# Performance work log

Hardware: AMD Instinct MI355X
Metric: run time of the kernel (lower is better)

Reference implementation:

```python
import jax, jax.numpy as jnp
import numpy as np

N_NODES = 300000   # cell instances
N_NETS  = 200000   # hyperedges (nets); each net has exactly one source/driver
E_SINK  = 1000000  # sink (node->net) pin edges
NODE_DIM, NET_DIM, EMB = 32, 16, 64
L, NUM_VN = 3, 1000
OUT_NODE, OUT_NET = 4, 4
SLOPE = 0.01  # torch leaky_relu default negative_slope


def leaky(x):
    return jnp.where(x >= 0, x, SLOPE * x)


def _lin(key, fan_in, fan_out):
    kw, kb = jax.random.split(key)
    b = 1.0 / np.sqrt(fan_in)
    W = jax.random.uniform(kw, (fan_in, fan_out), jnp.float32, -b, b)
    bb = jax.random.uniform(kb, (fan_out,), jnp.float32, -b, b)
    return W, bb


def setup_inputs() -> dict:
    key = jax.random.key(0)
    ks = iter(jax.random.split(key, 64))
    d = {}
    d["node_features"] = jax.random.normal(next(ks), (N_NODES, NODE_DIM), jnp.float32)
    d["net_features"] = jax.random.normal(next(ks), (N_NETS, NET_DIM), jnp.float32)
    d["src_nodes"] = jax.random.randint(next(ks), (N_NETS,), 0, N_NODES)   # driver node of net i
    d["sink_nodes"] = jax.random.randint(next(ks), (E_SINK,), 0, N_NODES)
    d["sink_nets"] = jax.random.randint(next(ks), (E_SINK,), 0, N_NETS)
    d["edge_weight"] = jax.random.uniform(next(ks), (E_SINK,), jnp.float32)
    d["batch"] = jax.random.randint(next(ks), (N_NODES,), 0, NUM_VN)       # node -> virtual node id
    # node / net encoders
    d["ne_W1"], d["ne_b1"] = _lin(next(ks), NODE_DIM, 2 * EMB)
    d["ne_W2"], d["ne_b2"] = _lin(next(ks), 2 * EMB, EMB)
    d["te_W1"], d["te_b1"] = _lin(next(ks), NET_DIM, EMB)
    d["te_W2"], d["te_b2"] = _lin(next(ks), EMB, EMB)
    d["vn_emb"] = jnp.zeros((EMB,), jnp.float32)  # torch: init.constant_(weight, 0)
    # HyperConv layers, stacked over L
    Wnet, bnet, Wnode, bnode = [], [], [], []
    for _ in range(L):
        W, b = _lin(next(ks), 3 * EMB, EMB); Wnet.append(W); bnet.append(b)
        W, b = _lin(next(ks), 2 * EMB, EMB); Wnode.append(W); bnode.append(b)
    d["conv_Wnet"] = jnp.stack(Wnet); d["conv_bnet"] = jnp.stack(bnet)
    d["conv_Wnode"] = jnp.stack(Wnode); d["conv_bnode"] = jnp.stack(bnode)
    # virtual-node MLPs (L-1 of them)
    vW1, vb1, vW2, vb2 = [], [], [], []
    for _ in range(L - 1):
        W, b = _lin(next(ks), EMB, EMB); vW1.append(W); vb1.append(b)
        W, b = _lin(next(ks), EMB, EMB); vW2.append(W); vb2.append(b)
    d["vn_W1"] = jnp.stack(vW1); d["vn_b1"] = jnp.stack(vb1)
    d["vn_W2"] = jnp.stack(vW2); d["vn_b2"] = jnp.stack(vb2)
    # output heads
    d["fc1n_W"], d["fc1n_b"] = _lin(next(ks), EMB, 256)
    d["fc2n_W"], d["fc2n_b"] = _lin(next(ks), 256, OUT_NODE)
    d["fc1e_W"], d["fc1e_b"] = _lin(next(ks), EMB, 64)
    d["fc2e_W"], d["fc2e_b"] = _lin(next(ks), 64, OUT_NET)
    return d


def _forward(node_features, net_features, edge_weight,
             ne_W1, ne_b1, ne_W2, ne_b2, te_W1, te_b1, te_W2, te_b2,
             vn_emb, conv_Wnet, conv_bnet, conv_Wnode, conv_bnode,
             vn_W1, vn_b1, vn_W2, vn_b2,
             fc1n_W, fc1n_b, fc2n_W, fc2n_b, fc1e_W, fc1e_b, fc2e_W, fc2e_b,
             src_nodes, sink_nodes, sink_nets, batch):
    h = leaky(node_features @ ne_W1 + ne_b1) @ ne_W2 + ne_b2   # [N, EMB]
    g = leaky(net_features @ te_W1 + te_b1) @ te_W2 + te_b2    # [M, EMB]
    w = edge_weight[:, None]
    vn = jnp.broadcast_to(vn_emb, (NUM_VN, EMB))               # embedding of all-zero indices
    for l in range(L):
        h = h + vn[batch]
        # node -> net (hyperedge) aggregation: driver message + weighted sink sum
        agg_src = h[src_nodes]                                             # [M, EMB]
        agg_sink = jax.ops.segment_sum(h[sink_nodes] * w, sink_nets, num_segments=N_NETS)
        g = jnp.concatenate([g, agg_src, agg_sink], axis=-1) @ conv_Wnet[l] + conv_bnet[l]
        # net -> node aggregation
        back = jax.ops.segment_sum(g, src_nodes, num_segments=N_NODES) \
             + jax.ops.segment_sum(g[sink_nets] * w, sink_nodes, num_segments=N_NODES)
        h = jnp.concatenate([h, back], axis=-1) @ conv_Wnode[l] + conv_bnode[l]
        h = leaky(h)
        g = leaky(g)
        if l < L - 1:
            pooled = jax.ops.segment_max(h, batch, num_segments=NUM_VN)   # global_max_pool
            tmp = pooled + vn
            vn = vn + (leaky(tmp @ vn_W1[l] + vn_b1[l]) @ vn_W2[l] + vn_b2[l])
    node_rep = jnp.abs(leaky(h @ fc1n_W + fc1n_b) @ fc2n_W + fc2n_b)
    net_rep = jnp.abs(leaky(g @ fc1e_W + fc1e_b) @ fc2e_W + fc2e_b)
    return node_rep, net_rep


def reference(node_features, net_features, edge_weight,
              ne_W1, ne_b1, ne_W2, ne_b2, te_W1, te_b1, te_W2, te_b2,
              vn_emb, conv_Wnet, conv_bnet, conv_Wnode, conv_bnode,
              vn_W1, vn_b1, vn_W2, vn_b2,
              fc1n_W, fc1n_b, fc2n_W, fc2n_b, fc1e_W, fc1e_b, fc2e_W, fc2e_b,
              src_nodes, sink_nodes, sink_nets, batch):
    return _forward(node_features, net_features, edge_weight,
                    ne_W1, ne_b1, ne_W2, ne_b2, te_W1, te_b1, te_W2, te_b2,
                    vn_emb, conv_Wnet, conv_bnet, conv_Wnode, conv_bnode,
                    vn_W1, vn_b1, vn_W2, vn_b2,
                    fc1n_W, fc1n_b, fc2n_W, fc2n_b, fc1e_W, fc1e_b, fc2e_W, fc2e_b,
                    src_nodes, sink_nodes, sink_nets, batch)
```

## Files before the change

### kernel.cpp

```cpp
#include <hip/hip_runtime.h>
#include <cstdint>

static constexpr int N_NODES = 300000;
static constexpr int N_NETS  = 200000;
static constexpr int E_SINK  = 1000000;
static constexpr int NODE_DIM = 32;
static constexpr int NET_DIM  = 16;
static constexpr int EMB = 64;
static constexpr int NUM_VN = 1000;
#define SLOPE 0.01f

typedef __attribute__((ext_vector_type(8))) short bhalf8;
typedef __attribute__((ext_vector_type(4))) float floatx4;
typedef unsigned short u16;

__device__ __forceinline__ float leaky(float x) { return x >= 0.f ? x : SLOPE * x; }

__device__ __forceinline__ unsigned bf16_rne(float x) {
    unsigned u = __float_as_uint(x);
    return (u + 0x7FFFu + ((u >> 16) & 1u)) >> 16;
}
__device__ __forceinline__ void split1(float x, u16& hh, u16& ll) {
    unsigned hb = bf16_rne(x);
    float fh = __uint_as_float(hb << 16);
    unsigned lb = bf16_rne(x - fh);
    hh = (u16)hb; ll = (u16)lb;
}

__device__ __forceinline__ void csplit8(const float* x, bhalf8& ah, bhalf8& al) {
#pragma unroll
    for (int e = 0; e < 8; ++e) {
        unsigned u = __float_as_uint(x[e]);
        ah[e] = (short)(u >> 16);
        float d = x[e] - __uint_as_float(u & 0xFFFF0000u);
        al[e] = (short)(__float_as_uint(d) >> 16);
    }
}
template<bool LK>
__device__ __forceinline__ void afrag32(const float* rowp, int kbase, bhalf8& ah, bhalf8& al) {
    float4 v0 = *(const float4*)(rowp + kbase);
    float4 v1 = *(const float4*)(rowp + kbase + 4);
    float x[8] = {v0.x, v0.y, v0.z, v0.w, v1.x, v1.y, v1.z, v1.w};
    if (LK) {
#pragma unroll
        for (int e = 0; e < 8; ++e) x[e] = leaky(x[e]);
    }
    csplit8(x, ah, al);
}
__device__ __forceinline__ void afragl(const float* tp, bhalf8& ah, bhalf8& al) {
    float4 v0 = *(const float4*)tp;
    float4 v1 = *(const float4*)(tp + 4);
    float x[8] = {v0.x, v0.y, v0.z, v0.w, v1.x, v1.y, v1.z, v1.w};
    csplit8(x, ah, al);
}

__device__ __forceinline__ floatx4 mm3(bhalf8 ah, bhalf8 al, bhalf8 wh, bhalf8 wl, floatx4 c) {
    c = __builtin_amdgcn_mfma_f32_16x16x32_bf16(ah, wh, c, 0, 0, 0);
    c = __builtin_amdgcn_mfma_f32_16x16x32_bf16(ah, wl, c, 0, 0, 0);
    c = __builtin_amdgcn_mfma_f32_16x16x32_bf16(al, wh, c, 0, 0, 0);
    return c;
}

static constexpr int OFF_NEW1 = 0;
static constexpr int OFF_NEW2 = 4096;
static constexpr int OFF_TEW1 = 12288;
static constexpr int OFF_TEW2 = 14336;
static constexpr int OFF_CWNET = 18432;
static constexpr int OFF_CWNODE = 55296;
static constexpr int OFF_FC1N = 79872;
static constexpr int OFF_FC1E = 96256;
static constexpr int W_TOTAL  = 100352;

__global__ void k_prep_w(const float* __restrict__ neW1, const float* __restrict__ neW2,
                         const float* __restrict__ teW1, const float* __restrict__ teW2,
                         const float* __restrict__ cWnet, const float* __restrict__ cWnode,
                         const float* __restrict__ fc1n, const float* __restrict__ fc1e,
                         u16* __restrict__ wfh, u16* __restrict__ wfl)
{
    int i = blockIdx.x * 256 + threadIdx.x;
    if (i >= W_TOTAL) return;
    int r, ncols, K; const float* src;
    if (i < OFF_NEW2)        { r = i;             src = neW1;  ncols = 128; K = 32; }
    else if (i < OFF_TEW1)   { r = i - OFF_NEW2;  src = neW2;  ncols = 64;  K = 128; }
    else if (i < OFF_TEW2)   { r = i - OFF_TEW1;  src = teW1;  ncols = 64;  K = 16; }
    else if (i < OFF_CWNET)  { r = i - OFF_TEW2;  src = teW2;  ncols = 64;  K = 64; }
    else if (i < OFF_CWNODE) { int t = i - OFF_CWNET;  int l = t / 12288; r = t % 12288;
                               src = cWnet + (size_t)l * 192 * 64; ncols = 64; K = 192; }
    else if (i < OFF_FC1N)   { int t = i - OFF_CWNODE; int l = t / 8192;  r = t % 8192;
                               src = cWnode + (size_t)l * 128 * 64; ncols = 64; K = 128; }
    else if (i < OFF_FC1E)   { r = i - OFF_FC1N;  src = fc1n;  ncols = 256; K = 64; }
    else                     { r = i - OFF_FC1E;  src = fc1e;  ncols = 64;  K = 64; }
    int e = r & 7, g = (r >> 3) & 3;
    int cidx = r >> 5;
    int col = cidx % ncols, kt = cidx / ncols;
    int k = kt * 32 + g * 8 + e;
    float v = (k < K) ? src[(size_t)k * ncols + col] : 0.f;
    u16 hh, ll; split1(v, hh, ll);
    wfh[i] = hh; wfl[i] = ll;
}

__device__ __forceinline__ bhalf8 ldw(const u16* p, int idx) {
    return *(const bhalf8*)(p + idx);
}

__global__ void k_hist_edges(const int* __restrict__ sink_nets, const int* __restrict__ sink_nodes,
                             int* __restrict__ cnt_net, int* __restrict__ cnt_node)
{
    int e = blockIdx.x * 256 + threadIdx.x;
    if (e >= E_SINK) return;
    atomicAdd(&cnt_net[sink_nets[e]], 1);
    atomicAdd(&cnt_node[sink_nodes[e]], 1);
}

__global__ void k_hist_misc(const int* __restrict__ src_nodes, const int* __restrict__ batch,
                            int* __restrict__ cnt_src, int* __restrict__ cnt_vn)
{
    int i = blockIdx.x * 256 + threadIdx.x;
    if (i < N_NETS) atomicAdd(&cnt_src[src_nodes[i]], 1);
    if (i < N_NODES) atomicAdd(&cnt_vn[batch[i]], 1);
}

__global__ void k_scan1(const int* __restrict__ cnt, int n, int* __restrict__ bsum) {
    __shared__ int s[256];
    int i = blockIdx.x * 256 + threadIdx.x;
    s[threadIdx.x] = (i < n) ? cnt[i] : 0;
    __syncthreads();
    for (int off = 128; off; off >>= 1) {
        if (threadIdx.x < off) s[threadIdx.x] += s[threadIdx.x + off];
        __syncthreads();
    }
    if (threadIdx.x == 0) bsum[blockIdx.x] = s[0];
}

__global__ void k_scan2(int* __restrict__ data, int n) {
    __shared__ int s[256];
    __shared__ int carry_s;
    int tid = threadIdx.x;
    if (tid == 0) carry_s = 0;
    __syncthreads();
    for (int base = 0; base < n; base += 256) {
        int i = base + tid;
        int v = (i < n) ? data[i] : 0;
        s[tid] = v;
        __syncthreads();
        for (int off = 1; off < 256; off <<= 1) {
            int t = (tid >= off) ? s[tid - off] : 0;
            __syncthreads();
            s[tid] += t;
            __syncthreads();
        }
        int excl = s[tid] - v + carry_s;
        if (i < n) data[i] = excl;
        __syncthreads();
        if (tid == 255) carry_s = excl + v;
        __syncthreads();
    }
}

__global__ void k_scan3(const int* __restrict__ cnt, int n, const int* __restrict__ bsum,
                        int* __restrict__ start) {
    __shared__ int s[256];
    int i = blockIdx.x * 256 + threadIdx.x;
    int v = (i < n) ? cnt[i] : 0;
    s[threadIdx.x] = v;
    __syncthreads();
    for (int off = 1; off < 256; off <<= 1) {
        int t = (threadIdx.x >= off) ? s[threadIdx.x - off] : 0;
        __syncthreads();
        s[threadIdx.x] += t;
        __syncthreads();
    }
    int excl = s[threadIdx.x] - v + bsum[blockIdx.x];
    if (i < n) start[i] = excl;
    if (i == n - 1) start[n] = excl + v;
}

__global__ void k_fill_edges(const int* __restrict__ sink_nets, const int* __restrict__ sink_nodes,
                             const float* __restrict__ ew,
                             const int* __restrict__ net_start, const int* __restrict__ node_start,
                             int* __restrict__ cur_net, int* __restrict__ cur_node,
                             int2* __restrict__ e_pack, int2* __restrict__ e2_pack)
{
    int e = blockIdx.x * 256 + threadIdx.x;
    if (e >= E_SINK) return;
    int tn = sink_nets[e], dn = sink_nodes[e];
    int wbits = __float_as_int(ew[e]);
    int p = net_start[tn] + atomicAdd(&cur_net[tn], 1);
    e_pack[p] = make_int2(dn, wbits);
    int q = node_start[dn] + atomicAdd(&cur_node[dn], 1);
    e2_pack[q] = make_int2(tn, wbits);
}

__global__ void k_fill_misc(const int* __restrict__ src_nodes, const int* __restrict__ batch,
                            const int* __restrict__ src_start, const int* __restrict__ vn_start,
                            int* __restrict__ cur_src, int* __restrict__ cur_vn,
                            int* __restrict__ s_net, int* __restrict__ b_node)
{
    int i = blockIdx.x * 256 + threadIdx.x;
    if (i < N_NETS) {
        int d = src_nodes[i];
        int p = src_start[d] + atomicAdd(&cur_src[d], 1);
        s_net[p] = i;
    }
    if (i < N_NODES) {
        int v = batch[i];
        int p = vn_start[v] + atomicAdd(&cur_vn[v], 1);
        b_node[p] = i;
    }
}

__global__ __launch_bounds__(256) void k_gather_agg(
    float* __restrict__ agg, const float* __restrict__ h,
    const int* __restrict__ net_start, const int2* __restrict__ e_pack)
{
    int w = (blockIdx.x * 256 + threadIdx.x) >> 6;
    if (w >= N_NETS) return;
    int lane = threadIdx.x & 63;
    int grp = lane >> 3, l8 = lane & 7;
    int j0 = net_start[w], j1 = net_start[w + 1];
    float a[8] = {0.f, 0.f, 0.f, 0.f, 0.f, 0.f, 0.f, 0.f};
    for (int j = j0 + grp; j < j1; j += 8) {
        int2 pk = e_pack[j];
        float wt = __int_as_float(pk.y);
        const float4* rp = (const float4*)(h + (size_t)pk.x * 64 + l8 * 8);
        float4 v0 = rp[0], v1 = rp[1];
        a[0] += wt * v0.x; a[1] += wt * v0.y; a[2] += wt * v0.z; a[3] += wt * v0.w;
        a[4] += wt * v1.x; a[5] += wt * v1.y; a[6] += wt * v1.z; a[7] += wt * v1.w;
    }
#pragma unroll
    for (int e = 0; e < 8; ++e) {
        a[e] += __shfl_xor(a[e], 8, 64);
        a[e] += __shfl_xor(a[e], 16, 64);
        a[e] += __shfl_xor(a[e], 32, 64);
    }
    if (grp == 0) {
        float4* op = (float4*)(agg + (size_t)w * 64 + l8 * 8);
        op[0] = make_float4(a[0], a[1], a[2], a[3]);
        op[1] = make_float4(a[4], a[5], a[6], a[7]);
    }
}

__global__ __launch_bounds__(256) void k_gather_back(
    float* __restrict__ back, const float* __restrict__ g,
    const int* __restrict__ src_start, const int* __restrict__ s_net,
    const int* __restrict__ node_start, const int2* __restrict__ e2_pack)
{
    int w = (blockIdx.x * 256 + threadIdx.x) >> 6;
    if (w >= N_NODES) return;
    int lane = threadIdx.x & 63;
    int grp = lane >> 3, l8 = lane & 7;
    float a[8] = {0.f, 0.f, 0.f, 0.f, 0.f, 0.f, 0.f, 0.f};
    int j0 = src_start[w], j1 = src_start[w + 1];
    for (int j = j0 + grp; j < j1; j += 8) {
        int idx = s_net[j];
        const float4* rp = (const float4*)(g + (size_t)idx * 64 + l8 * 8);
        float4 v0 = rp[0], v1 = rp[1];
        a[0] += v0.x; a[1] += v0.y; a[2] += v0.z; a[3] += v0.w;
        a[4] += v1.x; a[5] += v1.y; a[6] += v1.z; a[7] += v1.w;
    }
    j0 = node_start[w]; j1 = node_start[w + 1];
    for (int j = j0 + grp; j < j1; j += 8) {
        int2 pk = e2_pack[j];
        float wt = __int_as_float(pk.y);
        const float4* rp = (const float4*)(g + (size_t)pk.x * 64 + l8 * 8);
        float4 v0 = rp[0], v1 = rp[1];
        a[0] += wt * v0.x; a[1] += wt * v0.y; a[2] += wt * v0.z; a[3] += wt * v0.w;
        a[4] += wt * v1.x; a[5] += wt * v1.y; a[6] += wt * v1.z; a[7] += wt * v1.w;
    }
#pragma unroll
    for (int e = 0; e < 8; ++e) {
        a[e] += __shfl_xor(a[e], 8, 64);
        a[e] += __shfl_xor(a[e], 16, 64);
        a[e] += __shfl_xor(a[e], 32, 64);
    }
    if (grp == 0) {
        float4* op = (float4*)(back + (size_t)w * 64 + l8 * 8);
        op[0] = make_float4(a[0], a[1], a[2], a[3]);
        op[1] = make_float4(a[4], a[5], a[6], a[7]);
    }
}

__global__ __launch_bounds__(256) void k_pool_gather(
    float* __restrict__ pooled, const float* __restrict__ h,
    const int* __restrict__ vn_start, const int* __restrict__ b_node)
{
    __shared__ float red[32][64];
    int tid = threadIdx.x;
    int grp = tid >> 3, l8 = tid & 7;
    int v = blockIdx.x;
    int j0 = vn_start[v], j1 = vn_start[v + 1];
    const float NEG = -__builtin_inff();
    float m[8] = {NEG, NEG, NEG, NEG, NEG, NEG, NEG, NEG};
    for (int j = j0 + grp; j < j1; j += 32) {
        int nd = b_node[j];
        const float4* rp = (const float4*)(h + (size_t)nd * 64 + l8 * 8);
        float4 v0 = rp[0], v1 = rp[1];
        m[0] = fmaxf(m[0], v0.x); m[1] = fmaxf(m[1], v0.y);
        m[2] = fmaxf(m[2], v0.z); m[3] = fmaxf(m[3], v0.w);
        m[4] = fmaxf(m[4], v1.x); m[5] = fmaxf(m[5], v1.y);
        m[6] = fmaxf(m[6], v1.z); m[7] = fmaxf(m[7], v1.w);
    }
#pragma unroll
    for (int e = 0; e < 8; ++e) red[grp][l8 * 8 + e] = m[e];
    __syncthreads();
    if (tid < 64) {
        float mm = red[0][tid];
#pragma unroll
        for (int q = 1; q < 32; ++q) mm = fmaxf(mm, red[q][tid]);
        pooled[(size_t)v * 64 + tid] = mm;
    }
}

__global__ __launch_bounds__(256) void k_node_enc(
    const float* __restrict__ x, const u16* __restrict__ wfh, const u16* __restrict__ wfl,
    const float* __restrict__ b1, const float* __restrict__ b2, float* __restrict__ h)
{
    __shared__ __align__(16) float t[64][132];
    int lane = threadIdx.x & 63, wid = threadIdx.x >> 6;
    int g16 = lane >> 4, l15 = lane & 15;
    int rbase = blockIdx.x * 64;
    int cs = wid * 16 + l15;

    bhalf8 W1H[2], W1L[2];
#pragma unroll
    for (int s = 0; s < 2; ++s) {
        int col = wid * 16 + s * 64 + l15;
        int fo = OFF_NEW1 + (col * 4 + g16) * 8;
        W1H[s] = ldw(wfh, fo); W1L[s] = ldw(wfl, fo);
    }
    bhalf8 W2H[4], W2L[4];
#pragma unroll
    for (int kt = 0; kt < 4; ++kt) {
        int fo = OFF_NEW2 + ((kt * 64 + cs) * 4 + g16) * 8;
        W2H[kt] = ldw(wfh, fo); W2L[kt] = ldw(wfl, fo);
    }

#pragma unroll
    for (int ms = 0; ms < 4; ++ms) {
        int r = min(rbase + ms * 16 + l15, N_NODES - 1);
        bhalf8 ah, al;
        afrag32<false>(x + (size_t)r * NODE_DIM, g16 * 8, ah, al);
#pragma unroll
        for (int s = 0; s < 2; ++s) {
            floatx4 acc = {0.f, 0.f, 0.f, 0.f};
            acc = mm3(ah, al, W1H[s], W1L[s], acc);
            int hc = wid * 16 + s * 64 + l15;
            float bb = b1[hc];
#pragma unroll
            for (int i = 0; i < 4; ++i)
                t[ms * 16 + g16 * 4 + i][hc] = leaky(acc[i] + bb);
        }
    }
    __syncthreads();

    float bias = b2[cs];
#pragma unroll
    for (int ms = 0; ms < 4; ++ms) {
        floatx4 acc = {0.f, 0.f, 0.f, 0.f};
#pragma unroll
        for (int kt = 0; kt < 4; ++kt) {
            bhalf8 ah, al;
            afragl(&t[ms * 16 + l15][kt * 32 + g16 * 8], ah, al);
            acc = mm3(ah, al, W2H[kt], W2L[kt], acc);
        }
#pragma unroll
        for (int i = 0; i < 4; ++i) {
            int r = rbase + ms * 16 + g16 * 4 + i;
            if (r < N_NODES) h[(size_t)r * 64 + cs] = acc[i] + bias;
        }
    }
}

__global__ __launch_bounds__(256) void k_net_enc(
    const float* __restrict__ x, const u16* __restrict__ wfh, const u16* __restrict__ wfl,
    const float* __restrict__ b1, const float* __restrict__ b2, float* __restrict__ g)
{
    __shared__ __align__(16) float t[64][68];
    int lane = threadIdx.x & 63, wid = threadIdx.x >> 6;
    int g16 = lane >> 4, l15 = lane & 15;
    int rbase = blockIdx.x * 64;
    int cs = wid * 16 + l15;

    int fo = OFF_TEW1 + (cs * 4 + g16) * 8;
    bhalf8 W1H = ldw(wfh, fo), W1L = ldw(wfl, fo);
    bhalf8 W2H[2], W2L[2];
#pragma unroll
    for (int kt = 0; kt < 2; ++kt) {
        int f2 = OFF_TEW2 + ((kt * 64 + cs) * 4 + g16) * 8;
        W2H[kt] = ldw(wfh, f2); W2L[kt] = ldw(wfl, f2);
    }

#pragma unroll
    for (int ms = 0; ms < 4; ++ms) {
        int r = min(rbase + ms * 16 + l15, N_NETS - 1);
        bhalf8 ah = {0,0,0,0,0,0,0,0}, al = {0,0,0,0,0,0,0,0};
        if (g16 < 2) afrag32<false>(x + (size_t)r * NET_DIM, g16 * 8, ah, al);
        floatx4 acc = {0.f, 0.f, 0.f, 0.f};
        acc = mm3(ah, al, W1H, W1L, acc);
        float bb = b1[cs];
#pragma unroll
        for (int i = 0; i < 4; ++i)
            t[ms * 16 + g16 * 4 + i][cs] = leaky(acc[i] + bb);
    }
    __syncthreads();

    float bias = b2[cs];
#pragma unroll
    for (int ms = 0; ms < 4; ++ms) {
        floatx4 acc = {0.f, 0.f, 0.f, 0.f};
#pragma unroll
        for (int kt = 0; kt < 2; ++kt) {
            bhalf8 ah, al;
            afragl(&t[ms * 16 + l15][kt * 32 + g16 * 8], ah, al);
            acc = mm3(ah, al, W2H[kt], W2L[kt], acc);
        }
#pragma unroll
        for (int i = 0; i < 4; ++i) {
            int r = rbase + ms * 16 + g16 * 4 + i;
            if (r < N_NETS) g[(size_t)r * 64 + cs] = acc[i] + bias;
        }
    }
}

__global__ void k_vn_init(float* __restrict__ vn, const float* __restrict__ vn_emb) {
    int idx = blockIdx.x * blockDim.x + threadIdx.x;
    if (idx < NUM_VN * EMB) vn[idx] = vn_emb[idx & 63];
}

__global__ void k_add_vn(float4* __restrict__ h4, const float* __restrict__ vn,
                         const int* __restrict__ batch) {
    int idx = blockIdx.x * blockDim.x + threadIdx.x;
    if (idx >= N_NODES * 16) return;
    int n = idx >> 4, c4 = idx & 15;
    const float4* vr = (const float4*)(vn + (size_t)batch[n] * 64);
    float4 hv = h4[idx], vv = vr[c4];
    h4[idx] = make_float4(hv.x + vv.x, hv.y + vv.y, hv.z + vv.z, hv.w + vv.w);
}

__global__ __launch_bounds__(256) void k_conv_net(
    float* __restrict__ g, const float* __restrict__ h, const float* __restrict__ s,
    const int* __restrict__ src,
    const u16* __restrict__ wfh, const u16* __restrict__ wfl, int wbase,
    const float* __restrict__ b, int lk0)
{
    int lane = threadIdx.x & 63, wid = threadIdx.x >> 6;
    int g16 = lane >> 4, l15 = lane & 15;
    int rbase = blockIdx.x * 64;
    int cs = wid * 16 + l15;

    bhalf8 WH[6], WL[6];
#pragma unroll
    for (int kt = 0; kt < 6; ++kt) {
        int fo = wbase + ((kt * 64 + cs) * 4 + g16) * 8;
        WH[kt] = ldw(wfh, fo); WL[kt] = ldw(wfl, fo);
    }

    bhalf8 GH[4][2], GL[4][2];
#pragma unroll
    for (int ms = 0; ms < 4; ++ms) {
        int r = min(rbase + ms * 16 + l15, N_NETS - 1);
        const float* rp = g + (size_t)r * 64;
#pragma unroll
        for (int kt = 0; kt < 2; ++kt) {
            if (lk0) afrag32<true>(rp, kt * 32 + g16 * 8, GH[ms][kt], GL[ms][kt]);
            else     afrag32<false>(rp, kt * 32 + g16 * 8, GH[ms][kt], GL[ms][kt]);
        }
    }
    __syncthreads();

    float bias = b[cs];
#pragma unroll
    for (int ms = 0; ms < 4; ++ms) {
        floatx4 acc = {0.f, 0.f, 0.f, 0.f};
#pragma unroll
        for (int kt = 0; kt < 2; ++kt) acc = mm3(GH[ms][kt], GL[ms][kt], WH[kt], WL[kt], acc);
        int ar = min(rbase + ms * 16 + l15, N_NETS - 1);
        const float* hp = h + (size_t)src[ar] * 64;
#pragma unroll
        for (int kt = 0; kt < 2; ++kt) {
            bhalf8 ah, al;
            afrag32<false>(hp, kt * 32 + g16 * 8, ah, al);
            acc = mm3(ah, al, WH[2 + kt], WL[2 + kt], acc);
        }
        const float* ap = s + (size_t)ar * 64;
#pragma unroll
        for (int kt = 0; kt < 2; ++kt) {
            bhalf8 ah, al;
            afrag32<false>(ap, kt * 32 + g16 * 8, ah, al);
            acc = mm3(ah, al, WH[4 + kt], WL[4 + kt], acc);
        }
#pragma unroll
        for (int i = 0; i < 4; ++i) {
            int r = rbase + ms * 16 + g16 * 4 + i;
            if (r < N_NETS) g[(size_t)r * 64 + cs] = acc[i] + bias;
        }
    }
}

__global__ __launch_bounds__(256) void k_conv_node(
    float* __restrict__ h, const float* __restrict__ s,
    const u16* __restrict__ wfh, const u16* __restrict__ wfl, int wbase,
    const float* __restrict__ b)
{
    int lane = threadIdx.x & 63, wid = threadIdx.x >> 6;
    int g16 = lane >> 4, l15 = lane & 15;
    int rbase = blockIdx.x * 64;
    int cs = wid * 16 + l15;

    bhalf8 WH[4], WL[4];
#pragma unroll
    for (int kt = 0; kt < 4; ++kt) {
        int fo = wbase + ((kt * 64 + cs) * 4 + g16) * 8;
        WH[kt] = ldw(wfh, fo); WL[kt] = ldw(wfl, fo);
    }

    bhalf8 HH[4][2], HL[4][2];
#pragma unroll
    for (int ms = 0; ms < 4; ++ms) {
        int r = min(rbase + ms * 16 + l15, N_NODES - 1);
        const float* rp = h + (size_t)r * 64;
#pragma unroll
        for (int kt = 0; kt < 2; ++kt)
            afrag32<false>(rp, kt * 32 + g16 * 8, HH[ms][kt], HL[ms][kt]);
    }
    __syncthreads();

    float bias = b[cs];
#pragma unroll
    for (int ms = 0; ms < 4; ++ms) {
        floatx4 acc = {0.f, 0.f, 0.f, 0.f};
#pragma unroll
        for (int kt = 0; kt < 2; ++kt) acc = mm3(HH[ms][kt], HL[ms][kt], WH[kt], WL[kt], acc);
        int ar = min(rbase + ms * 16 + l15, N_NODES - 1);
        const float* bp = s + (size_t)ar * 64;
#pragma unroll
        for (int kt = 0; kt < 2; ++kt) {
            bhalf8 ah, al;
            afrag32<false>(bp, kt * 32 + g16 * 8, ah, al);
            acc = mm3(ah, al, WH[2 + kt], WL[2 + kt], acc);
        }
#pragma unroll
        for (int i = 0; i < 4; ++i) {
            int r = rbase + ms * 16 + g16 * 4 + i;
            if (r < N_NODES) h[(size_t)r * 64 + cs] = leaky(acc[i] + bias);
        }
    }
}

__global__ __launch_bounds__(256) void k_vn_update(
    float* __restrict__ vn, const float* __restrict__ pooled,
    const float* __restrict__ W1, const float* __restrict__ b1,
    const float* __restrict__ W2, const float* __restrict__ b2)
{
    int wv = threadIdx.x >> 6, lane = threadIdx.x & 63;
    int v = blockIdx.x * 4 + wv;
    if (v >= NUM_VN) return;
    float p = pooled[(size_t)v * 64 + lane];
    float vv = vn[v * 64 + lane];
    float tmp = p + vv;
    float t1 = b1[lane];
#pragma unroll 16
    for (int k = 0; k < 64; ++k) t1 += __shfl(tmp, k, 64) * W1[k * 64 + lane];
    t1 = leaky(t1);
    float t2 = b2[lane];
#pragma unroll 16
    for (int k = 0; k < 64; ++k) t2 += __shfl(t1, k, 64) * W2[k * 64 + lane];
    vn[v * 64 + lane] = vv + t2;
}

__global__ __launch_bounds__(256) void k_fc_node(
    float* __restrict__ out, const float* __restrict__ h,
    const u16* __restrict__ wfh, const u16* __restrict__ wfl,
    const float* __restrict__ b1, const float* __restrict__ W2, const float* __restrict__ b2)
{
    __shared__ float red[4][64][4];
    int lane = threadIdx.x & 63, wid = threadIdx.x >> 6;
    int g16 = lane >> 4, l15 = lane & 15;
    int rbase = blockIdx.x * 64;

    bhalf8 W1H[4][2], W1L[4][2];
    float4 w2v[4];
    float b1v[4];
#pragma unroll
    for (int s = 0; s < 4; ++s) {
        int hc = wid * 16 + s * 64 + l15;
#pragma unroll
        for (int kt = 0; kt < 2; ++kt) {
            int fo = OFF_FC1N + ((kt * 256 + hc) * 4 + g16) * 8;
            W1H[s][kt] = ldw(wfh, fo); W1L[s][kt] = ldw(wfl, fo);
        }
        w2v[s] = *(const float4*)(W2 + hc * 4);
        b1v[s] = b1[hc];
    }

#pragma unroll
    for (int ms = 0; ms < 4; ++ms) {
        int r = min(rbase + ms * 16 + l15, N_NODES - 1);
        bhalf8 ah[2], al[2];
#pragma unroll
        for (int kt = 0; kt < 2; ++kt)
            afrag32<false>(h + (size_t)r * 64, kt * 32 + g16 * 8, ah[kt], al[kt]);
        float po[4][4] = {{0.f,0.f,0.f,0.f},{0.f,0.f,0.f,0.f},{0.f,0.f,0.f,0.f},{0.f,0.f,0.f,0.f}};
#pragma unroll
        for (int s = 0; s < 4; ++s) {
            floatx4 acc = {0.f, 0.f, 0.f, 0.f};
#pragma unroll
            for (int kt = 0; kt < 2; ++kt) acc = mm3(ah[kt], al[kt], W1H[s][kt], W1L[s][kt], acc);
#pragma unroll
            for (int i = 0; i < 4; ++i) {
                float act = leaky(acc[i] + b1v[s]);
                po[i][0] += act * w2v[s].x;
                po[i][1] += act * w2v[s].y;
                po[i][2] += act * w2v[s].z;
                po[i][3] += act * w2v[s].w;
            }
        }
#pragma unroll
        for (int i = 0; i < 4; ++i)
#pragma unroll
            for (int o = 0; o < 4; ++o) {
                po[i][o] += __shfl_xor(po[i][o], 1, 64);
                po[i][o] += __shfl_xor(po[i][o], 2, 64);
                po[i][o] += __shfl_xor(po[i][o], 4, 64);
                po[i][o] += __shfl_xor(po[i][o], 8, 64);
            }
        if (l15 == 0) {
#pragma unroll
            for (int i = 0; i < 4; ++i)
#pragma unroll
                for (int o = 0; o < 4; ++o)
                    red[wid][ms * 16 + g16 * 4 + i][o] = po[i][o];
        }
    }
    __syncthreads();
    int tid = threadIdx.x;
    int row = tid >> 2, o = tid & 3;
    float sum = red[0][row][o] + red[1][row][o] + red[2][row][o] + red[3][row][o];
    int r = rbase + row;
    if (r < N_NODES) out[(size_t)r * 4 + o] = fabsf(sum + b2[o]);
}

__global__ __launch_bounds__(256) void k_fc_net(
    float* __restrict__ out, const float* __restrict__ g,
    const u16* __restrict__ wfh, const u16* __restrict__ wfl,
    const float* __restrict__ b1, const float* __restrict__ W2, const float* __restrict__ b2)
{
    __shared__ float red[4][64][4];
    int lane = threadIdx.x & 63, wid = threadIdx.x >> 6;
    int g16 = lane >> 4, l15 = lane & 15;
    int rbase = blockIdx.x * 64;
    int cs = wid * 16 + l15;

    bhalf8 W1H[2], W1L[2];
#pragma unroll
    for (int kt = 0; kt < 2; ++kt) {
        int fo = OFF_FC1E + ((kt * 64 + cs) * 4 + g16) * 8;
        W1H[kt] = ldw(wfh, fo); W1L[kt] = ldw(wfl, fo);
    }
    float4 w2v = *(const float4*)(W2 + cs * 4);
    float b1v = b1[cs];

#pragma unroll
    for (int ms = 0; ms < 4; ++ms) {
        int r = min(rbase + ms * 16 + l15, N_NETS - 1);
        bhalf8 ah[2], al[2];
#pragma unroll
        for (int kt = 0; kt < 2; ++kt)
            afrag32<true>(g + (size_t)r * 64, kt * 32 + g16 * 8, ah[kt], al[kt]);
        floatx4 acc = {0.f, 0.f, 0.f, 0.f};
#pragma unroll
        for (int kt = 0; kt < 2; ++kt) acc = mm3(ah[kt], al[kt], W1H[kt], W1L[kt], acc);
        float po[4][4];
#pragma unroll
        for (int i = 0; i < 4; ++i) {
            float act = leaky(acc[i] + b1v);
            po[i][0] = act * w2v.x;
            po[i][1] = act * w2v.y;
            po[i][2] = act * w2v.z;
            po[i][3] = act * w2v.w;
        }
#pragma unroll
        for (int i = 0; i < 4; ++i)
#pragma unroll
            for (int o = 0; o < 4; ++o) {
                po[i][o] += __shfl_xor(po[i][o], 1, 64);
                po[i][o] += __shfl_xor(po[i][o], 2, 64);
                po[i][o] += __shfl_xor(po[i][o], 4, 64);
                po[i][o] += __shfl_xor(po[i][o], 8, 64);
            }
        if (l15 == 0) {
#pragma unroll
            for (int i = 0; i < 4; ++i)
#pragma unroll
                for (int o = 0; o < 4; ++o)
                    red[wid][ms * 16 + g16 * 4 + i][o] = po[i][o];
        }
    }
    __syncthreads();
    int tid = threadIdx.x;
    int row = tid >> 2, o = tid & 3;
    float sum = red[0][row][o] + red[1][row][o] + red[2][row][o] + red[3][row][o];
    int r = rbase + row;
    if (r < N_NETS) out[(size_t)r * 4 + o] = fabsf(sum + b2[o]);
}

extern "C" void kernel_launch(void* const* d_in, const int* in_sizes, int n_in,
                              void* d_out, int out_size, void* d_ws, size_t ws_size,
                              hipStream_t stream)
{
    const float* node_features = (const float*)d_in[0];
    const float* net_features  = (const float*)d_in[1];
    const int*   src_nodes     = (const int*)d_in[2];
    const int*   sink_nodes    = (const int*)d_in[3];
    const int*   sink_nets     = (const int*)d_in[4];
    const float* edge_weight   = (const float*)d_in[5];
    const int*   batch         = (const int*)d_in[6];
    const float* ne_W1 = (const float*)d_in[7];
    const float* ne_b1 = (const float*)d_in[8];
    const float* ne_W2 = (const float*)d_in[9];
    const float* ne_b2 = (const float*)d_in[10];
    const float* te_W1 = (const float*)d_in[11];
    const float* te_b1 = (const float*)d_in[12];
    const float* te_W2 = (const float*)d_in[13];
    const float* te_b2 = (const float*)d_in[14];
    const float* vn_emb = (const float*)d_in[15];
    const float* conv_Wnet  = (const float*)d_in[16];
    const float* conv_bnet  = (const float*)d_in[17];
    const float* conv_Wnode = (const float*)d_in[18];
    const float* conv_bnode = (const float*)d_in[19];
    const float* vn_W1 = (const float*)d_in[20];
    const float* vn_b1 = (const float*)d_in[21];
    const float* vn_W2 = (const float*)d_in[22];
    const float* vn_b2 = (const float*)d_in[23];
    const float* fc1n_W = (const float*)d_in[24];
    const float* fc1n_b = (const float*)d_in[25];
    const float* fc2n_W = (const float*)d_in[26];
    const float* fc2n_b = (const float*)d_in[27];
    const float* fc1e_W = (const float*)d_in[28];
    const float* fc1e_b = (const float*)d_in[29];
    const float* fc2e_W = (const float*)d_in[30];
    const float* fc2e_b = (const float*)d_in[31];

    float* out_node = (float*)d_out;
    float* out_net  = out_node + (size_t)N_NODES * 4;

    char* wsp = (char*)d_ws;
    size_t used = 0;
    auto alloc = [&](size_t bytes) -> char* {
        char* r = wsp + used;
        used += (bytes + 255) & ~(size_t)255;
        return r;
    };
    float* h  = (float*)alloc((size_t)N_NODES * 64 * 4);
    float* g  = (float*)alloc((size_t)N_NETS * 64 * 4);
    float* s  = (float*)alloc((size_t)N_NODES * 64 * 4);
    u16* wfh  = (u16*)alloc((size_t)W_TOTAL * 2);
    u16* wfl  = (u16*)alloc((size_t)W_TOTAL * 2);
    float* vn     = (float*)alloc((size_t)NUM_VN * EMB * 4);
    float* pooled = (float*)alloc((size_t)NUM_VN * EMB * 4);
    int* net_start  = (int*)alloc((size_t)(N_NETS + 1) * 4);
    int* node_start = (int*)alloc((size_t)(N_NODES + 1) * 4);
    int* src_start  = (int*)alloc((size_t)(N_NODES + 1) * 4);
    int* vn_start   = (int*)alloc((size_t)(NUM_VN + 1) * 4);
    int2* e_pack  = (int2*)alloc((size_t)E_SINK * 8);
    int2* e2_pack = (int2*)alloc((size_t)E_SINK * 8);
    int* s_net  = (int*)alloc((size_t)N_NETS * 4);
    int* b_node = (int*)alloc((size_t)N_NODES * 4);
    const int CNT_TOTAL = N_NETS + N_NODES + N_NODES + NUM_VN;
    int* cnt  = (int*)alloc((size_t)CNT_TOTAL * 4);
    int* bsum = (int*)alloc(2048 * 4);
    int* cnt_net  = cnt;
    int* cnt_node = cnt + N_NETS;
    int* cnt_src  = cnt_node + N_NODES;
    int* cnt_vn   = cnt_src + N_NODES;

    const int nodeTiles = (N_NODES + 63) / 64;
    const int netTiles  = (N_NETS + 63) / 64;
    const int vnBlocks  = (NUM_VN + 3) / 4;
    const int vnElemBlocks  = (NUM_VN * EMB + 255) / 256;
    const int addVnBlocks  = (N_NODES * 16 + 255) / 256;
    const int edgeThreadBlocks = (E_SINK + 255) / 256;
    const int miscThreadBlocks = (N_NODES + 255) / 256;
    const int netWaveBlocks  = (N_NETS + 3) / 4;
    const int nodeWaveBlocks = (N_NODES + 3) / 4;
    const int prepBlocks = (W_TOTAL + 255) / 256;

    hipMemsetAsync(cnt, 0, (size_t)CNT_TOTAL * sizeof(int), stream);
    k_hist_edges<<<edgeThreadBlocks, 256, 0, stream>>>(sink_nets, sink_nodes, cnt_net, cnt_node);
    k_hist_misc<<<miscThreadBlocks, 256, 0, stream>>>(src_nodes, batch, cnt_src, cnt_vn);

    auto scan = [&](int* cnt_arr, int n, int* start_arr) {
        int nb = (n + 255) / 256;
        k_scan1<<<nb, 256, 0, stream>>>(cnt_arr, n, bsum);
        k_scan2<<<1, 256, 0, stream>>>(bsum, nb);
        k_scan3<<<nb, 256, 0, stream>>>(cnt_arr, n, bsum, start_arr);
    };
    scan(cnt_net, N_NETS, net_start);
    scan(cnt_node, N_NODES, node_start);
    scan(cnt_src, N_NODES, src_start);
    scan(cnt_vn, NUM_VN, vn_start);

    hipMemsetAsync(cnt, 0, (size_t)CNT_TOTAL * sizeof(int), stream);
    k_fill_edges<<<edgeThreadBlocks, 256, 0, stream>>>(sink_nets, sink_nodes, edge_weight,
        net_start, node_start, cnt_net, cnt_node, e_pack, e2_pack);
    k_fill_misc<<<miscThreadBlocks, 256, 0, stream>>>(src_nodes, batch, src_start, vn_start,
        cnt_src, cnt_vn, s_net, b_node);

    k_prep_w<<<prepBlocks, 256, 0, stream>>>(ne_W1, ne_W2, te_W1, te_W2,
                                             conv_Wnet, conv_Wnode, fc1n_W, fc1e_W, wfh, wfl);
    k_node_enc<<<nodeTiles, 256, 0, stream>>>(node_features, wfh, wfl, ne_b1, ne_b2, h);
    k_net_enc<<<netTiles, 256, 0, stream>>>(net_features, wfh, wfl, te_b1, te_b2, g);
    k_vn_init<<<vnElemBlocks, 256, 0, stream>>>(vn, vn_emb);

    for (int l = 0; l < 3; ++l) {
        k_add_vn<<<addVnBlocks, 256, 0, stream>>>((float4*)h, vn, batch);

        k_gather_agg<<<netWaveBlocks, 256, 0, stream>>>(s, h, net_start, e_pack);
        k_conv_net<<<netTiles, 256, 0, stream>>>(g, h, s, src_nodes,
            wfh, wfl, OFF_CWNET + l * 12288, conv_bnet + (size_t)l * 64, l > 0 ? 1 : 0);

        k_gather_back<<<nodeWaveBlocks, 256, 0, stream>>>(s, g,
            src_start, s_net, node_start, e2_pack);
        k_conv_node<<<nodeTiles, 256, 0, stream>>>(h, s,
            wfh, wfl, OFF_CWNODE + l * 8192, conv_bnode + (size_t)l * 64);

        if (l < 2) {
            k_pool_gather<<<NUM_VN, 256, 0, stream>>>(pooled, h, vn_start, b_node);
            k_vn_update<<<vnBlocks, 256, 0, stream>>>(vn, pooled,
                vn_W1 + (size_t)l * 64 * 64, vn_b1 + (size_t)l * 64,
                vn_W2 + (size_t)l * 64 * 64, vn_b2 + (size_t)l * 64);
        }
    }

    k_fc_node<<<nodeTiles, 256, 0, stream>>>(out_node, h, wfh, wfl, fc1n_b, fc2n_W, fc2n_b);
    k_fc_net<<<netTiles, 256, 0, stream>>>(out_net, g, wfh, wfl, fc1e_b, fc2e_W, fc2e_b);
}
```

Baseline: 1.679 ms.

## Run node head second layer on MFMA via LDS staging; drop counter re-memset

The node output head's 256->4 projection moves off scalar FMAs and shuffle reductions. The hidden activations are now staged in shared memory in two halves, and the projection runs as split-bf16 MFMAs against fc2 weights that are pre-split in the weight prep kernel. Separately, the fill kernels now count down the histogram counters with atomicSub, so the second memset of the counter buffer can be dropped. The MFMA path wastes 12 of 16 output columns and adds LDS traffic and block barriers.

```diff
diff --git a/kernel.cpp b/kernel.cpp
--- a/kernel.cpp
+++ b/kernel.cpp
@@ -69,12 +69,15 @@
 static constexpr int OFF_CWNODE = 55296;
 static constexpr int OFF_FC1N = 79872;
 static constexpr int OFF_FC1E = 96256;
-static constexpr int W_TOTAL  = 100352;
+static constexpr int OFF_FC2N = 100352;
+static constexpr int OFF_FC2E = 101376;
+static constexpr int W_TOTAL  = 101632;
 
 __global__ void k_prep_w(const float* __restrict__ neW1, const float* __restrict__ neW2,
                          const float* __restrict__ teW1, const float* __restrict__ teW2,
                          const float* __restrict__ cWnet, const float* __restrict__ cWnode,
                          const float* __restrict__ fc1n, const float* __restrict__ fc1e,
+                         const float* __restrict__ fc2n, const float* __restrict__ fc2e,
                          u16* __restrict__ wfh, u16* __restrict__ wfl)
 {
     int i = blockIdx.x * 256 + threadIdx.x;
@@ -89,7 +92,9 @@
     else if (i < OFF_FC1N)   { int t = i - OFF_CWNODE; int l = t / 8192;  r = t % 8192;
                                src = cWnode + (size_t)l * 128 * 64; ncols = 64; K = 128; }
     else if (i < OFF_FC1E)   { r = i - OFF_FC1N;  src = fc1n;  ncols = 256; K = 64; }
-    else                     { r = i - OFF_FC1E;  src = fc1e;  ncols = 64;  K = 64; }
+    else if (i < OFF_FC2N)   { r = i - OFF_FC1E;  src = fc1e;  ncols = 64;  K = 64; }
+    else if (i < OFF_FC2E)   { r = i - OFF_FC2N;  src = fc2n;  ncols = 4;   K = 256; }
+    else                     { r = i - OFF_FC2E;  src = fc2e;  ncols = 4;   K = 64; }
     int e = r & 7, g = (r >> 3) & 3;
     int cidx = r >> 5;
     int col = cidx % ncols, kt = cidx / ncols;
@@ -178,33 +183,33 @@
 __global__ void k_fill_edges(const int* __restrict__ sink_nets, const int* __restrict__ sink_nodes,
                              const float* __restrict__ ew,
                              const int* __restrict__ net_start, const int* __restrict__ node_start,
-                             int* __restrict__ cur_net, int* __restrict__ cur_node,
+                             int* __restrict__ cnt_net, int* __restrict__ cnt_node,
                              int2* __restrict__ e_pack, int2* __restrict__ e2_pack)
 {
     int e = blockIdx.x * 256 + threadIdx.x;
     if (e >= E_SINK) return;
     int tn = sink_nets[e], dn = sink_nodes[e];
     int wbits = __float_as_int(ew[e]);
-    int p = net_start[tn] + atomicAdd(&cur_net[tn], 1);
+    int p = net_start[tn] + atomicSub(&cnt_net[tn], 1) - 1;
     e_pack[p] = make_int2(dn, wbits);
-    int q = node_start[dn] + atomicAdd(&cur_node[dn], 1);
+    int q = node_start[dn] + atomicSub(&cnt_node[dn], 1) - 1;
     e2_pack[q] = make_int2(tn, wbits);
 }
 
 __global__ void k_fill_misc(const int* __restrict__ src_nodes, const int* __restrict__ batch,
                             const int* __restrict__ src_start, const int* __restrict__ vn_start,
-                            int* __restrict__ cur_src, int* __restrict__ cur_vn,
+                            int* __restrict__ cnt_src, int* __restrict__ cnt_vn,
                             int* __restrict__ s_net, int* __restrict__ b_node)
 {
     int i = blockIdx.x * 256 + threadIdx.x;
     if (i < N_NETS) {
         int d = src_nodes[i];
-        int p = src_start[d] + atomicAdd(&cur_src[d], 1);
+        int p = src_start[d] + atomicSub(&cnt_src[d], 1) - 1;
         s_net[p] = i;
     }
     if (i < N_NODES) {
         int v = batch[i];
-        int p = vn_start[v] + atomicAdd(&cur_vn[v], 1);
+        int p = vn_start[v] + atomicSub(&cnt_vn[v], 1) - 1;
         b_node[p] = i;
     }
 }
@@ -571,15 +576,14 @@
 __global__ __launch_bounds__(256) void k_fc_node(
     float* __restrict__ out, const float* __restrict__ h,
     const u16* __restrict__ wfh, const u16* __restrict__ wfl,
-    const float* __restrict__ b1, const float* __restrict__ W2, const float* __restrict__ b2)
-{
-    __shared__ float red[4][64][4];
+    const float* __restrict__ b1, const float* __restrict__ b2)
+{
+    __shared__ __align__(16) float t[64][132];
     int lane = threadIdx.x & 63, wid = threadIdx.x >> 6;
     int g16 = lane >> 4, l15 = lane & 15;
     int rbase = blockIdx.x * 64;
 
     bhalf8 W1H[4][2], W1L[4][2];
-    float4 w2v[4];
     float b1v[4];
 #pragma unroll
     for (int s = 0; s < 4; ++s) {
@@ -589,55 +593,59 @@
             int fo = OFF_FC1N + ((kt * 256 + hc) * 4 + g16) * 8;
             W1H[s][kt] = ldw(wfh, fo); W1L[s][kt] = ldw(wfl, fo);
         }
-        w2v[s] = *(const float4*)(W2 + hc * 4);
         b1v[s] = b1[hc];
     }
-
-#pragma unroll
-    for (int ms = 0; ms < 4; ++ms) {
-        int r = min(rbase + ms * 16 + l15, N_NODES - 1);
-        bhalf8 ah[2], al[2];
-#pragma unroll
-        for (int kt = 0; kt < 2; ++kt)
-            afrag32<false>(h + (size_t)r * 64, kt * 32 + g16 * 8, ah[kt], al[kt]);
-        float po[4][4] = {{0.f,0.f,0.f,0.f},{0.f,0.f,0.f,0.f},{0.f,0.f,0.f,0.f},{0.f,0.f,0.f,0.f}};
-#pragma unroll
-        for (int s = 0; s < 4; ++s) {
-            floatx4 acc = {0.f, 0.f, 0.f, 0.f};
-#pragma unroll
-            for (int kt = 0; kt < 2; ++kt) acc = mm3(ah[kt], al[kt], W1H[s][kt], W1L[s][kt], acc);
-#pragma unroll
-            for (int i = 0; i < 4; ++i) {
-                float act = leaky(acc[i] + b1v[s]);
-                po[i][0] += act * w2v[s].x;
-                po[i][1] += act * w2v[s].y;
-                po[i][2] += act * w2v[s].z;
-                po[i][3] += act * w2v[s].w;
+    bhalf8 W2H[8], W2L[8];
+    const bhalf8 zfr = {0,0,0,0,0,0,0,0};
+#pragma unroll
+    for (int kt = 0; kt < 8; ++kt) {
+        if (l15 < 4) {
+            int fo = OFF_FC2N + ((kt * 4 + l15) * 4 + g16) * 8;
+            W2H[kt] = ldw(wfh, fo); W2L[kt] = ldw(wfl, fo);
+        } else { W2H[kt] = zfr; W2L[kt] = zfr; }
+    }
+
+    floatx4 oacc = {0.f, 0.f, 0.f, 0.f};
+#pragma unroll
+    for (int c = 0; c < 2; ++c) {
+#pragma unroll
+        for (int ms = 0; ms < 4; ++ms) {
+            int r = min(rbase + ms * 16 + l15, N_NODES - 1);
+            bhalf8 ah[2], al[2];
+#pragma unroll
+            for (int kt = 0; kt < 2; ++kt)
+                afrag32<false>(h + (size_t)r * 64, kt * 32 + g16 * 8, ah[kt], al[kt]);
+#pragma unroll
+            for (int sl = 0; sl < 2; ++sl) {
+                int s = c * 2 + sl;
+                floatx4 acc = {0.f, 0.f, 0.f, 0.f};
+#pragma unroll
+                for (int kt = 0; kt < 2; ++kt)
+                    acc = mm3(ah[kt], al[kt], W1H[s][kt], W1L[s][kt], acc);
+                int hl = wid * 16 + sl * 64 + l15;
+#pragma unroll
+                for (int i = 0; i < 4; ++i)
+                    t[ms * 16 + g16 * 4 + i][hl] = leaky(acc[i] + b1v[s]);
             }
         }
-#pragma unroll
-        for (int i = 0; i < 4; ++i)
-#pragma unroll
-            for (int o = 0; o < 4; ++o) {
-                po[i][o] += __shfl_xor(po[i][o], 1, 64);
-                po[i][o] += __shfl_xor(po[i][o], 2, 64);
-                po[i][o] += __shfl_xor(po[i][o], 4, 64);
-                po[i][o] += __shfl_xor(po[i][o], 8, 64);
-            }
-        if (l15 == 0) {
-#pragma unroll
-            for (int i = 0; i < 4; ++i)
-#pragma unroll
-                for (int o = 0; o < 4; ++o)
-                    red[wid][ms * 16 + g16 * 4 + i][o] = po[i][o];
-        }
-    }
-    __syncthreads();
-    int tid = threadIdx.x;
-    int row = tid >> 2, o = tid & 3;
-    float sum = red[0][row][o] + red[1][row][o] + red[2][row][o] + red[3][row][o];
-    int r = rbase + row;
-    if (r < N_NODES) out[(size_t)r * 4 + o] = fabsf(sum + b2[o]);
+        __syncthreads();
+#pragma unroll
+        for (int ktl = 0; ktl < 4; ++ktl) {
+            bhalf8 ah, al;
+            afragl(&t[wid * 16 + l15][ktl * 32 + g16 * 8], ah, al);
+            int ktg = c * 4 + ktl;
+            oacc = mm3(ah, al, W2H[ktg], W2L[ktg], oacc);
+        }
+        __syncthreads();
+    }
+    if (l15 < 4) {
+        float bo = b2[l15];
+#pragma unroll
+        for (int i = 0; i < 4; ++i) {
+            int r = rbase + wid * 16 + g16 * 4 + i;
+            if (r < N_NODES) out[(size_t)r * 4 + l15] = fabsf(oacc[i] + bo);
+        }
+    }
 }
 
 __global__ __launch_bounds__(256) void k_fc_net(
@@ -800,14 +808,14 @@
     scan(cnt_src, N_NODES, src_start);
     scan(cnt_vn, NUM_VN, vn_start);
 
-    hipMemsetAsync(cnt, 0, (size_t)CNT_TOTAL * sizeof(int), stream);
     k_fill_edges<<<edgeThreadBlocks, 256, 0, stream>>>(sink_nets, sink_nodes, edge_weight,
         net_start, node_start, cnt_net, cnt_node, e_pack, e2_pack);
     k_fill_misc<<<miscThreadBlocks, 256, 0, stream>>>(src_nodes, batch, src_start, vn_start,
         cnt_src, cnt_vn, s_net, b_node);
 
     k_prep_w<<<prepBlocks, 256, 0, stream>>>(ne_W1, ne_W2, te_W1, te_W2,
-                                             conv_Wnet, conv_Wnode, fc1n_W, fc1e_W, wfh, wfl);
+                                             conv_Wnet, conv_Wnode, fc1n_W, fc1e_W,
+                                             fc2n_W, fc2e_W, wfh, wfl);
     k_node_enc<<<nodeTiles, 256, 0, stream>>>(node_features, wfh, wfl, ne_b1, ne_b2, h);
     k_net_enc<<<netTiles, 256, 0, stream>>>(net_features, wfh, wfl, te_b1, te_b2, g);
     k_vn_init<<<vnElemBlocks, 256, 0, stream>>>(vn, vn_emb);
@@ -832,6 +840,6 @@
         }
     }
 
-    k_fc_node<<<nodeTiles, 256, 0, stream>>>(out_node, h, wfh, wfl, fc1n_b, fc2n_W, fc2n_b);
+    k_fc_node<<<nodeTiles, 256, 0, stream>>>(out_node, h, wfh, wfl, fc1n_b, fc2n_b);
     k_fc_net<<<netTiles, 256, 0, stream>>>(out_net, g, wfh, wfl, fc1e_b, fc2e_W, fc2e_b);
 }
```

New measurement: 1.752 ms. +4.4%, slower.
